# Performance work log

Hardware: AMD Instinct MI355X
Metric: run time of the kernel (lower is better)

The kernel has to match this reference:

```python
import jax, jax.numpy as jnp
import numpy as np

N_NODES = 16000
N_EDGES = 128000
IN_FEAT = 1024   # nb_iprs
OUT_FEAT = 1024  # RelGraphConv out / embed_dim
N_RELS = 7
NB_GOS = 4096


def setup_inputs() -> dict:
    key = jax.random.key(0)
    ks = jax.random.split(key, 9)
    feat = jax.random.normal(ks[0], (N_NODES, IN_FEAT), dtype=jnp.float32)
    src = jax.random.randint(ks[1], (N_EDGES,), 0, N_NODES, dtype=jnp.int32)
    dst = jax.random.randint(ks[2], (N_EDGES,), 0, N_NODES, dtype=jnp.int32)
    etypes = jax.random.randint(ks[3], (N_EDGES,), 0, N_RELS, dtype=jnp.int32)
    # RelGraphConv params (regularizer=None): per-relation weight, self-loop weight, bias
    s = 1.0 / np.sqrt(IN_FEAT)
    W_rel = jax.random.uniform(ks[4], (N_RELS, IN_FEAT, OUT_FEAT), dtype=jnp.float32, minval=-s, maxval=s)
    W_loop = jax.random.uniform(ks[5], (IN_FEAT, OUT_FEAT), dtype=jnp.float32, minval=-s, maxval=s)
    bias = jnp.zeros((OUT_FEAT,), dtype=jnp.float32)
    # GO embeddings, init U(-k, k) with k = sqrt(1/embed_dim)
    k = 1.0 / np.sqrt(OUT_FEAT)
    go_embed = jax.random.uniform(ks[6], (NB_GOS, OUT_FEAT), dtype=jnp.float32, minval=-k, maxval=k)
    go_rad = jax.random.uniform(ks[7], (NB_GOS, 1), dtype=jnp.float32, minval=-k, maxval=k)
    return {"feat": feat, "src": src, "dst": dst, "etypes": etypes,
            "W_rel": W_rel, "W_loop": W_loop, "bias": bias,
            "go_embed": go_embed, "go_rad": go_rad}


def reference(feat, src, dst, etypes, W_rel, W_loop, bias, go_embed, go_rad):
    n = feat.shape[0]
    # RelGraphConv (sum aggregation, self-loop, bias, no activation):
    # message on edge e: feat[src[e]] @ W_rel[etypes[e]]; by linearity, first
    # segment-sum source features per (dst, rel), then one batched GEMM.
    x_src = feat[src]                                   # [E, in]
    seg = dst.astype(jnp.int32) * N_RELS + etypes       # combined (dst, rel) id
    agg = jax.ops.segment_sum(x_src, seg, num_segments=n * N_RELS)
    agg = agg.reshape(n, N_RELS, IN_FEAT)               # [N, R, in]
    h = jnp.einsum('nri,rio->no', agg, W_rel) + feat @ W_loop + bias  # [N, out]
    # scoring: sigmoid(x @ E_go^T + |rad|)
    logits = jax.nn.sigmoid(h @ go_embed.T + jnp.abs(go_rad).reshape(1, -1))
    return logits
```

## Files before the change

kernel.cpp:

```cpp
#include <hip/hip_runtime.h>
#include <math.h>

#define N_NODES 16000
#define N_EDGES 128000
#define KDIM 1024
#define N_RELS 7
#define NB_GOS 4096
#define KCAT (KDIM * (N_RELS + 1))
#define MPAD 16128

#define BM 128
#define BN 128
#define BK 32
#define CAP2 (N_EDGES + N_RELS * BM)
#define NTILE_E (CAP2 / BM)

typedef __attribute__((ext_vector_type(8))) short bf16x8;
typedef __attribute__((ext_vector_type(8))) unsigned short u16x8;
typedef __attribute__((ext_vector_type(4))) float f32x4;

__device__ __forceinline__ unsigned short f2bf(float f) {
    union { float f; unsigned int u; } v; v.f = f;
    unsigned int u = v.u + 0x7FFFu + ((v.u >> 16) & 1u);
    return (unsigned short)(u >> 16);
}

__device__ __forceinline__ void gload16(const void* g, void* lds) {
    __builtin_amdgcn_global_load_lds(
        (const __attribute__((address_space(1))) unsigned int*)g,
        (__attribute__((address_space(3))) unsigned int*)lds, 16, 0, 0);
}

__device__ __forceinline__ void wg_barrier() {
    __builtin_amdgcn_sched_barrier(0);
    asm volatile("s_barrier" ::: "memory");
    __builtin_amdgcn_sched_barrier(0);
}


__global__ __launch_bounds__(256) void conv_bf16(const float* __restrict__ in,
                                                 unsigned short* __restrict__ out, int n8) {
    int i = blockIdx.x * 256 + threadIdx.x;
    if (i >= n8) return;
    const float4* in4 = (const float4*)in;
    float4 x = in4[2 * i], y = in4[2 * i + 1];
    u16x8 o;
    o[0] = f2bf(x.x); o[1] = f2bf(x.y); o[2] = f2bf(x.z); o[3] = f2bf(x.w);
    o[4] = f2bf(y.x); o[5] = f2bf(y.y); o[6] = f2bf(y.z); o[7] = f2bf(y.w);
    *(u16x8*)&out[(size_t)i * 8] = o;
}

__global__ __launch_bounds__(256) void conv_cat(const float* __restrict__ in,
                                                unsigned short* __restrict__ Acat) {
    int i = blockIdx.x * 256 + threadIdx.x;
    if (i >= N_NODES * (KDIM / 8)) return;
    int n = i >> 7, c8 = (i & 127) * 8;
    const float4* in4 = (const float4*)(in + (size_t)n * KDIM + c8);
    float4 x = in4[0], y = in4[1];
    u16x8 o;
    o[0] = f2bf(x.x); o[1] = f2bf(x.y); o[2] = f2bf(x.z); o[3] = f2bf(x.w);
    o[4] = f2bf(y.x); o[5] = f2bf(y.y); o[6] = f2bf(y.z); o[7] = f2bf(y.w);
    *(u16x8*)&Acat[(size_t)n * KCAT + c8] = o;
}

__global__ void transpose_w(const float* __restrict__ Wrel,
                            const float* __restrict__ Wloop,
                            unsigned short* __restrict__ WrelT,
                            unsigned short* __restrict__ WloopT) {
    __shared__ float t[32][33];
    int z = blockIdx.z;
    const float* src = (z < N_RELS) ? Wrel + (size_t)z * KDIM * KDIM : Wloop;
    unsigned short* dst = (z < N_RELS) ? WrelT + (size_t)z * KDIM * KDIM : WloopT;
    int tx = threadIdx.x, ty = threadIdx.y;
    int x = blockIdx.x * 32 + tx;
    int y0 = blockIdx.y * 32;
    #pragma unroll
    for (int j = 0; j < 4; j++)
        t[ty + 8 * j][tx] = src[(size_t)(y0 + ty + 8 * j) * KDIM + x];
    __syncthreads();
    #pragma unroll
    for (int j = 0; j < 4; j++) {
        int n = blockIdx.x * 32 + ty + 8 * j;
        dst[(size_t)n * KDIM + y0 + tx] = f2bf(t[tx][ty + 8 * j]);
    }
}

__global__ void transpose_cat(const float* __restrict__ Wrel,
                              const float* __restrict__ Wloop,
                              unsigned short* __restrict__ BT) {
    __shared__ float t[32][33];
    int z = blockIdx.z;
    const float* src = (z == 0) ? Wloop : Wrel + (size_t)(z - 1) * KDIM * KDIM;
    int tx = threadIdx.x, ty = threadIdx.y;
    int x = blockIdx.x * 32 + tx;
    int y0 = blockIdx.y * 32;
    #pragma unroll
    for (int j = 0; j < 4; j++)
        t[ty + 8 * j][tx] = src[(size_t)(y0 + ty + 8 * j) * KDIM + x];
    __syncthreads();
    #pragma unroll
    for (int j = 0; j < 4; j++) {
        int o = blockIdx.x * 32 + ty + 8 * j;
        BT[(size_t)o * KCAT + z * KDIM + y0 + tx] = f2bf(t[tx][ty + 8 * j]);
    }
}


__global__ void zero_ints(int* p, int n) {
    int i = blockIdx.x * 256 + threadIdx.x;
    if (i < n) p[i] = 0;
}

__global__ void hist_dst(const int* __restrict__ dst, int* cnt) {
    int e = blockIdx.x * 256 + threadIdx.x;
    if (e < N_EDGES) atomicAdd(&cnt[dst[e]], 1);
}

__global__ __launch_bounds__(1024) void scan_offs(const int* __restrict__ cnt,
                                                  int* __restrict__ offs) {
    __shared__ int part[1024];
    int t = threadIdx.x;
    int base = t * 16;
    int local[16];
    int s = 0;
    if (base < N_NODES) {
        #pragma unroll
        for (int j = 0; j < 16; j++) { local[j] = cnt[base + j]; s += local[j]; }
    }
    part[t] = s;
    __syncthreads();
    for (int d = 1; d < 1024; d <<= 1) {
        int v = (t >= d) ? part[t - d] : 0;
        __syncthreads();
        part[t] += v;
        __syncthreads();
    }
    if (base < N_NODES) {
        int ex = (t == 0) ? 0 : part[t - 1];
        #pragma unroll
        for (int j = 0; j < 16; j++) { offs[base + j] = ex; ex += local[j]; }
        if (base + 16 == N_NODES) offs[N_NODES] = ex;
    }
}

__global__ void scatter_dst(const int* __restrict__ src, const int* __restrict__ dst,
                            const int* __restrict__ et, const int* __restrict__ offs,
                            int* cursor, int* __restrict__ se) {
    int e = blockIdx.x * 256 + threadIdx.x;
    if (e < N_EDGES) {
        int d = dst[e];
        int p = atomicAdd(&cursor[d], 1);
        se[offs[d] + p] = (src[e] << 3) | et[e];
    }
}

__global__ __launch_bounds__(256) void aggregate(const float* __restrict__ feat,
                                                 const int* __restrict__ offs,
                                                 const int* __restrict__ se,
                                                 unsigned short* __restrict__ Acat) {
    int n = blockIdx.x;
    int t = threadIdx.x;
    int e0 = offs[n], e1 = offs[n + 1];
    float4 a0 = {0,0,0,0}, a1 = a0, a2 = a0, a3 = a0, a4 = a0, a5 = a0, a6 = a0;
    const float4* f4 = (const float4*)feat;
    for (int i = e0; i < e1; i++) {
        int v = se[i];
        int s = v >> 3, r = v & 7;
        float4 x = f4[(size_t)s * (KDIM / 4) + t];
        #define ADD4(a) { a.x += x.x; a.y += x.y; a.z += x.z; a.w += x.w; }
        switch (r) {
            case 0: ADD4(a0) break; case 1: ADD4(a1) break;
            case 2: ADD4(a2) break; case 3: ADD4(a3) break;
            case 4: ADD4(a4) break; case 5: ADD4(a5) break;
            default: ADD4(a6) break;
        }
        #undef ADD4
    }
    unsigned short* row = Acat + (size_t)n * KCAT + KDIM;
    #define ST4(rr, a) { ushort4 o; o.x = f2bf(a.x); o.y = f2bf(a.y); \
                         o.z = f2bf(a.z); o.w = f2bf(a.w); \
                         *(ushort4*)(row + rr * KDIM + t * 4) = o; }
    ST4(0, a0) ST4(1, a1) ST4(2, a2) ST4(3, a3) ST4(4, a4) ST4(5, a5) ST4(6, a6)
    #undef ST4
}


template<int MODE>
__global__ __launch_bounds__(512, 2) void gemm256(
    const unsigned short* __restrict__ A,
    const unsigned short* __restrict__ BT,
    const float* __restrict__ br,
    float* __restrict__ out, int kd)
{
    __shared__ unsigned short As[2][256 * 64];
    __shared__ unsigned short Bs[2][256 * 64];

    const int tid = threadIdx.x;
    const int l = tid & 63, w = tid >> 6;
    const int wm = w >> 2, wn = w & 3;

    const int nwg = gridDim.x * gridDim.y;
    const int b = blockIdx.y * gridDim.x + blockIdx.x;
    const int q8 = nwg >> 3, r8 = nwg & 7;
    const int xcd = b & 7, idx = b >> 3;
    const int wg = (xcd < r8 ? xcd * (q8 + 1) : r8 * (q8 + 1) + (xcd - r8) * q8) + idx;
    const int m0 = (wg / gridDim.x) * 256;
    const int n0 = (wg % gridDim.x) * 256;

    const int NT = kd >> 6;

    const int rr = tid >> 3;
    const int cc = (tid & 7) ^ (rr & 7);

    auto stageA = [&](int dbuf, int kt, int half) {
        #pragma unroll
        for (int j = 0; j < 2; j++) {
            unsigned short* lp = &As[dbuf][(size_t)(w * 8 + j * 128 + half * 64) * 64];
            const unsigned short* gp = A + (size_t)(m0 + rr + j * 128 + half * 64) * kd
                                         + kt * 64 + cc * 8;
            gload16(gp, lp);
        }
    };
    auto stageB = [&](int dbuf, int kt, int half) {
        #pragma unroll
        for (int j = 0; j < 2; j++) {
            unsigned short* lp = &Bs[dbuf][(size_t)(w * 8 + j * 64 + half * 128) * 64];
            const unsigned short* gp = BT + (size_t)(n0 + rr + j * 64 + half * 128) * kd
                                          + kt * 64 + cc * 8;
            gload16(gp, lp);
        }
    };

    stageB(0, 0, 0); stageA(0, 0, 0); stageB(0, 0, 1); stageA(0, 0, 1);
    if (NT > 1) {
        stageB(1, 1, 0); stageA(1, 1, 0); stageB(1, 1, 1);
        asm volatile("s_waitcnt vmcnt(6)" ::: "memory");
    } else {
        asm volatile("s_waitcnt vmcnt(0)" ::: "memory");
    }
    wg_barrier();

    f32x4 acc[8][4] = {};

    for (int t = 0; t < NT; t++) {
        const int buf = t & 1;
        bf16x8 bfr[4][2];
        #pragma unroll
        for (int q = 0; q < 4; q++) {
            bf16x8 afr[2][2];
            if (q == 0) {
                #pragma unroll
                for (int nj = 0; nj < 4; nj++)
                    #pragma unroll
                    for (int ks = 0; ks < 2; ks++) {
                        int row = wn * 64 + nj * 16 + (l & 15);
                        int ch = (ks * 4 + (l >> 4)) ^ (l & 7);
                        bfr[nj][ks] = *(const bf16x8*)&Bs[buf][row * 64 + ch * 8];
                    }
            }
            #pragma unroll
            for (int i = 0; i < 2; i++)
                #pragma unroll
                for (int ks = 0; ks < 2; ks++) {
                    int row = wm * 128 + (2 * q + i) * 16 + (l & 15);
                    int ch = (ks * 4 + (l >> 4)) ^ (l & 7);
                    afr[i][ks] = *(const bf16x8*)&As[buf][row * 64 + ch * 8];
                }
            if (q == 0)      { if (t + 1 < NT) stageA(buf ^ 1, t + 1, 1); }
            else if (q == 1) { if (t + 2 < NT) stageB(buf, t + 2, 0); }
            else if (q == 2) { if (t + 2 < NT) stageA(buf, t + 2, 0); }
            else             { if (t + 2 < NT) stageB(buf, t + 2, 1); }
            wg_barrier();
            __builtin_amdgcn_s_setprio(1);
            #pragma unroll
            for (int i = 0; i < 2; i++)
                #pragma unroll
                for (int nj = 0; nj < 4; nj++)
                    #pragma unroll
                    for (int ks = 0; ks < 2; ks++)
                        acc[2 * q + i][nj] = __builtin_amdgcn_mfma_f32_16x16x32_bf16(
                            afr[i][ks], bfr[nj][ks], acc[2 * q + i][nj], 0, 0, 0);
            __builtin_amdgcn_s_setprio(0);
            if (q == 3) {
                if (t + 2 < NT) asm volatile("s_waitcnt vmcnt(6)" ::: "memory");
                else            asm volatile("s_waitcnt vmcnt(0)" ::: "memory");
            }
            wg_barrier();
        }
    }

    const int cl = l & 15, rh = (l >> 4) * 4;
    float brv[4];
    #pragma unroll
    for (int nj = 0; nj < 4; nj++) brv[nj] = br[n0 + wn * 64 + nj * 16 + cl];
    #pragma unroll
    for (int mi = 0; mi < 8; mi++) {
        #pragma unroll
        for (int r4 = 0; r4 < 4; r4++) {
            const int row = m0 + wm * 128 + mi * 16 + rh + r4;
            if (MODE == 2 && row >= N_NODES) continue;
            #pragma unroll
            for (int nj = 0; nj < 4; nj++) {
                const int col = n0 + wn * 64 + nj * 16 + cl;
                float x = acc[mi][nj][r4];
                if (MODE == 0) {
                    out[(size_t)row * KDIM + col] = x + brv[nj];
                } else {
                    x += fabsf(brv[nj]);
                    out[(size_t)row * (size_t)NB_GOS + col] = 1.0f / (1.0f + __expf(-x));
                }
            }
        }
    }
}


__global__ void init_buckets(int* cnt, int* cursor, int* bucket) {
    int i = blockIdx.x * 256 + threadIdx.x;
    if (i < 8) { cnt[i] = 0; cursor[i] = 0; }
    if (i < CAP2) bucket[i] = -1;
}

__global__ __launch_bounds__(256) void count_etypes(const int* __restrict__ et, int* cnt) {
    __shared__ int lc[N_RELS];
    if (threadIdx.x < N_RELS) lc[threadIdx.x] = 0;
    __syncthreads();
    int e = blockIdx.x * 256 + threadIdx.x;
    if (e < N_EDGES) atomicAdd(&lc[et[e]], 1);
    __syncthreads();
    if (threadIdx.x < N_RELS) atomicAdd(&cnt[threadIdx.x], lc[threadIdx.x]);
}

__global__ void calc_offsets(const int* __restrict__ cnt, int* offs) {
    if (blockIdx.x == 0 && threadIdx.x == 0) {
        int acc = 0;
        offs[0] = 0;
        for (int r = 0; r < N_RELS; r++) {
            acc += ((cnt[r] + BM - 1) / BM) * BM;
            offs[r + 1] = acc;
        }
    }
}

__global__ __launch_bounds__(256) void scatter_edges(const int* __restrict__ et,
                                                     const int* __restrict__ offs,
                                                     int* cursor, int* bucket) {
    __shared__ int lc[N_RELS];
    __shared__ int lbase[N_RELS];
    if (threadIdx.x < N_RELS) lc[threadIdx.x] = 0;
    __syncthreads();
    int e = blockIdx.x * 256 + threadIdx.x;
    int r = 0, my = 0;
    bool valid = (e < N_EDGES);
    if (valid) { r = et[e]; my = atomicAdd(&lc[r], 1); }
    __syncthreads();
    if (threadIdx.x < N_RELS)
        lbase[threadIdx.x] = atomicAdd(&cursor[threadIdx.x], lc[threadIdx.x]);
    __syncthreads();
    if (valid) bucket[offs[r] + lbase[r] + my] = e;
}

template<int MODE>
__global__ __launch_bounds__(256) void mfma_gemm(
    const unsigned short* __restrict__ A,
    const unsigned short* __restrict__ BT,
    const float* __restrict__ br,
    float* __restrict__ out,
    const int* __restrict__ src,
    const int* __restrict__ dst,
    const int* __restrict__ bucket,
    const int* __restrict__ offs,
    int kd)
{
    __shared__ unsigned short As[BM * BK];
    __shared__ unsigned short Bs[BN * BK];
    __shared__ int s_src[BM];
    __shared__ int s_dst[BM];

    const int tid = threadIdx.x;
    const int l = tid & 63;
    const int w = tid >> 6;
    const int wr = w >> 1, wc = w & 1;

    const int nwg = gridDim.x * gridDim.y;
    const int b = blockIdx.y * gridDim.x + blockIdx.x;
    const int cpx = nwg >> 3;
    const int swz = (b & 7) * cpx + (b >> 3);
    const int n0 = (swz / gridDim.y) * BN;
    const int m0 = (swz % gridDim.y) * BM;

    const unsigned short* Bb = BT;
    if (MODE == 1) {
        int rel = -1;
        #pragma unroll
        for (int q = 0; q < N_RELS; q++)
            if (m0 >= offs[q] && m0 < offs[q + 1]) rel = q;
        if (rel < 0) return;
        Bb = BT + (size_t)rel * KDIM * KDIM;
        if (tid < BM) {
            int e = bucket[m0 + tid];
            s_src[tid] = (e >= 0) ? src[e] : -1;
            s_dst[tid] = (e >= 0) ? dst[e] : -1;
        }
        __syncthreads();
    }

    f32x4 acc[4][4] = {};

    const int s0 = tid, s1 = tid + 256;
    const int r0 = s0 >> 2, kc0 = (s0 & 3) * 8;
    const int r1 = s1 >> 2, kc1 = (s1 & 3) * 8;
    unsigned short* ldsA0 = As + (w * 64) * 8;
    unsigned short* ldsA1 = As + (w * 64 + 256) * 8;
    unsigned short* ldsB0 = Bs + (w * 64) * 8;
    unsigned short* ldsB1 = Bs + (w * 64 + 256) * 8;

    size_t arow0, arow1;
    if (MODE == 1) {
        int sr0 = s_src[r0]; arow0 = (sr0 < 0) ? 0 : (size_t)sr0;
        int sr1 = s_src[r1]; arow1 = (sr1 < 0) ? 0 : (size_t)sr1;
    } else {
        arow0 = (size_t)(m0 + r0);
        arow1 = (size_t)(m0 + r1);
    }
    const size_t brow0 = (size_t)(n0 + r0), brow1 = (size_t)(n0 + r1);

    const int fa = (wr * 64 + (l & 15)) * BK + (l >> 4) * 8;
    const int fb = (wc * 64 + (l & 15)) * BK + (l >> 4) * 8;

    for (int k0 = 0; k0 < kd; k0 += BK) {
        gload16(A + arow0 * kd + k0 + kc0, ldsA0);
        gload16(A + arow1 * kd + k0 + kc1, ldsA1);
        gload16(Bb + brow0 * kd + k0 + kc0, ldsB0);
        gload16(Bb + brow1 * kd + k0 + kc1, ldsB1);
        __syncthreads();

        bf16x8 a[4], bfr[4];
        #pragma unroll
        for (int mi = 0; mi < 4; mi++)
            a[mi] = *(const bf16x8*)&As[fa + mi * 16 * BK];
        #pragma unroll
        for (int nj = 0; nj < 4; nj++)
            bfr[nj] = *(const bf16x8*)&Bs[fb + nj * 16 * BK];
        #pragma unroll
        for (int mi = 0; mi < 4; mi++)
            #pragma unroll
            for (int nj = 0; nj < 4; nj++)
                acc[mi][nj] = __builtin_amdgcn_mfma_f32_16x16x32_bf16(a[mi], bfr[nj], acc[mi][nj], 0, 0, 0);
        __syncthreads();
    }

    const int cl = l & 15, rh = (l >> 4) * 4;
    #pragma unroll
    for (int mi = 0; mi < 4; mi++) {
        #pragma unroll
        for (int r4 = 0; r4 < 4; r4++) {
            const int row = wr * 64 + mi * 16 + rh + r4;
            if (MODE == 1) {
                const int d = s_dst[row];
                if (d >= 0) {
                    #pragma unroll
                    for (int nj = 0; nj < 4; nj++) {
                        const int col = n0 + wc * 64 + nj * 16 + cl;
                        atomicAdd(&out[(size_t)d * KDIM + col], acc[mi][nj][r4]);
                    }
                }
            } else if (MODE == 0) {
                #pragma unroll
                for (int nj = 0; nj < 4; nj++) {
                    const int col = n0 + wc * 64 + nj * 16 + cl;
                    out[(size_t)(m0 + row) * KDIM + col] = acc[mi][nj][r4] + br[col];
                }
            } else {
                #pragma unroll
                for (int nj = 0; nj < 4; nj++) {
                    const int col = n0 + wc * 64 + nj * 16 + cl;
                    float x = acc[mi][nj][r4] + fabsf(br[col]);
                    out[(size_t)(m0 + row) * (size_t)NB_GOS + col] = 1.0f / (1.0f + expf(-x));
                }
            }
        }
    }
}


extern "C" void kernel_launch(void* const* d_in, const int* in_sizes, int n_in,
                              void* d_out, int out_size, void* d_ws, size_t ws_size,
                              hipStream_t stream) {
    const float* feat   = (const float*)d_in[0];
    const int*   src    = (const int*)d_in[1];
    const int*   dst    = (const int*)d_in[2];
    const int*   etypes = (const int*)d_in[3];
    const float* W_rel  = (const float*)d_in[4];
    const float* W_loop = (const float*)d_in[5];
    const float* bias   = (const float*)d_in[6];
    const float* go_emb = (const float*)d_in[7];
    const float* go_rad = (const float*)d_in[8];
    float* out = (float*)d_out;

    const size_t ACAT_B = (size_t)MPAD * KCAT * 2;
    const size_t H_B    = (size_t)MPAD * KDIM * 4;
    const size_t BTC_B  = (size_t)KDIM * KCAT * 2;
    const size_t GOB_B  = (size_t)NB_GOS * KDIM * 2;
    const size_t CNT_B  = 16384 * 4;
    const size_t NEED   = ACAT_B + H_B + BTC_B + GOB_B + 3 * CNT_B + (size_t)N_EDGES * 4;

    if (ws_size >= NEED) {
        char* p = (char*)d_ws;
        unsigned short* Acat  = (unsigned short*)p;  p += ACAT_B;
        float*          h     = (float*)p;           p += H_B;
        unsigned short* BTcat = (unsigned short*)p;  p += BTC_B;
        unsigned short* gob   = (unsigned short*)p;  p += GOB_B;
        int* cnt    = (int*)p;                       p += CNT_B;
        int* cursor = (int*)p;                       p += CNT_B;
        int* offs   = (int*)p;                       p += CNT_B;
        int* se     = (int*)p;
        unsigned short* hb = (unsigned short*)d_ws;

        zero_ints<<<(2 * 16384 + 255) / 256, 256, 0, stream>>>(cnt, 2 * 16384);
        conv_cat<<<(N_NODES * (KDIM / 8) + 255) / 256, 256, 0, stream>>>(feat, Acat);
        conv_bf16<<<(NB_GOS * KDIM / 8 + 255) / 256, 256, 0, stream>>>(go_emb, gob, NB_GOS * KDIM / 8);
        {
            dim3 g(KDIM / 32, KDIM / 32, N_RELS + 1), bb(32, 8);
            transpose_cat<<<g, bb, 0, stream>>>(W_rel, W_loop, BTcat);
        }
        hist_dst<<<(N_EDGES + 255) / 256, 256, 0, stream>>>(dst, cnt);
        scan_offs<<<1, 1024, 0, stream>>>(cnt, offs);
        scatter_dst<<<(N_EDGES + 255) / 256, 256, 0, stream>>>(src, dst, etypes, offs, cursor, se);
        aggregate<<<N_NODES, 256, 0, stream>>>(feat, offs, se, Acat);

        {
            dim3 g(KDIM / 256, MPAD / 256);
            gemm256<0><<<g, 512, 0, stream>>>(Acat, BTcat, bias, h, KCAT);
        }
        conv_bf16<<<(N_NODES * KDIM / 8 + 255) / 256, 256, 0, stream>>>(h, hb, N_NODES * KDIM / 8);
        {
            dim3 g(NB_GOS / 256, MPAD / 256);
            gemm256<2><<<g, 512, 0, stream>>>(hb, gob, go_rad, out, KDIM);
        }
        return;
    }

    char* p = (char*)d_ws;
    float* h            = (float*)p;            p += (size_t)N_NODES * KDIM * 4;
    unsigned short* fb  = (unsigned short*)p;   p += (size_t)N_NODES * KDIM * 2;
    unsigned short* wrT = (unsigned short*)p;   p += (size_t)N_RELS * KDIM * KDIM * 2;
    unsigned short* wlT = (unsigned short*)p;   p += (size_t)KDIM * KDIM * 2;
    unsigned short* gob = (unsigned short*)p;   p += (size_t)NB_GOS * KDIM * 2;
    int* cnt    = (int*)p;
    int* cursor = cnt + 8;
    int* offs   = cursor + 8;
    int* bucket = offs + 16;

    conv_bf16<<<(N_NODES * KDIM / 8 + 255) / 256, 256, 0, stream>>>(feat, fb, N_NODES * KDIM / 8);
    conv_bf16<<<(NB_GOS * KDIM / 8 + 255) / 256, 256, 0, stream>>>(go_emb, gob, NB_GOS * KDIM / 8);
    {
        dim3 g(KDIM / 32, KDIM / 32, N_RELS + 1), bb(32, 8);
        transpose_w<<<g, bb, 0, stream>>>(W_rel, W_loop, wrT, wlT);
    }
    init_buckets<<<(CAP2 + 255) / 256, 256, 0, stream>>>(cnt, cursor, bucket);
    count_etypes<<<(N_EDGES + 255) / 256, 256, 0, stream>>>(etypes, cnt);
    calc_offsets<<<1, 64, 0, stream>>>(cnt, offs);
    scatter_edges<<<(N_EDGES + 255) / 256, 256, 0, stream>>>(etypes, offs, cursor, bucket);
    {
        dim3 g(KDIM / BN, N_NODES / BM);
        mfma_gemm<0><<<g, 256, 0, stream>>>(fb, wlT, bias, h, nullptr, nullptr, nullptr, nullptr, KDIM);
    }
    {
        dim3 g(KDIM / BN, NTILE_E);
        mfma_gemm<1><<<g, 256, 0, stream>>>(fb, wrT, nullptr, h, src, dst, bucket, offs, KDIM);
    }
    conv_bf16<<<(N_NODES * KDIM / 8 + 255) / 256, 256, 0, stream>>>(h, fb, N_NODES * KDIM / 8);
    {
        dim3 g(NB_GOS / BN, N_NODES / BM);
        mfma_gemm<2><<<g, 256, 0, stream>>>(fb, gob, go_rad, out, nullptr, nullptr, nullptr, nullptr, KDIM);
    }
}
```

Baseline: 681.0 us.

## Restructure GEMM main loop into eight quadrant phases and fuse bf16 epilogue

Rewrites the gemm256 main loop to process two K-tiles per iteration in eight phases, each computing one 64x32 quadrant of the warp tile with interleaved async global->LDS staging and a changed B-tile row mapping. It also makes the first GEMM write its output directly as bf16, which removes the separate fp32 h buffer and the conv_bf16 pass. The finer phasing aims to overlap loads with MFMA more evenly, at the cost of more barriers and an assumption that NT is even. The epilogue fusion saves a full read/write of h.

```diff
diff --git a/kernel.cpp b/kernel.cpp
--- a/kernel.cpp
+++ b/kernel.cpp
@@ -29,12 +29,6 @@
     __builtin_amdgcn_global_load_lds(
         (const __attribute__((address_space(1))) unsigned int*)g,
         (__attribute__((address_space(3))) unsigned int*)lds, 16, 0, 0);
-}
-
-__device__ __forceinline__ void wg_barrier() {
-    __builtin_amdgcn_sched_barrier(0);
-    asm volatile("s_barrier" ::: "memory");
-    __builtin_amdgcn_sched_barrier(0);
 }
 
 
@@ -190,7 +184,7 @@
     const unsigned short* __restrict__ A,
     const unsigned short* __restrict__ BT,
     const float* __restrict__ br,
-    float* __restrict__ out, int kd)
+    void* __restrict__ outv, int kd)
 {
     __shared__ unsigned short As[2][256 * 64];
     __shared__ unsigned short Bs[2][256 * 64];
@@ -198,6 +192,7 @@
     const int tid = threadIdx.x;
     const int l = tid & 63, w = tid >> 6;
     const int wm = w >> 2, wn = w & 3;
+    const int lrow = l & 15, lhi = l >> 4, lx = l & 7;
 
     const int nwg = gridDim.x * gridDim.y;
     const int b = blockIdx.y * gridDim.x + blockIdx.x;
@@ -208,6 +203,7 @@
     const int n0 = (wg % gridDim.x) * 256;
 
     const int NT = kd >> 6;
+    const int NI = NT >> 1;
 
     const int rr = tid >> 3;
     const int cc = (tid & 7) ^ (rr & 7);
@@ -224,70 +220,74 @@
     auto stageB = [&](int dbuf, int kt, int half) {
         #pragma unroll
         for (int j = 0; j < 2; j++) {
-            unsigned short* lp = &Bs[dbuf][(size_t)(w * 8 + j * 64 + half * 128) * 64];
-            const unsigned short* gp = BT + (size_t)(n0 + rr + j * 64 + half * 128) * kd
+            const int brow = (w & 3) * 8 + (w >> 2) * 64 + j * 128 + half * 32;
+            unsigned short* lp = &Bs[dbuf][(size_t)brow * 64];
+            const unsigned short* gp = BT + (size_t)(n0 + (rr & 31) + (rr >> 5) * 64
+                                                     + j * 128 + half * 32) * kd
                                           + kt * 64 + cc * 8;
             gload16(gp, lp);
         }
     };
 
-    stageB(0, 0, 0); stageA(0, 0, 0); stageB(0, 0, 1); stageA(0, 0, 1);
-    if (NT > 1) {
-        stageB(1, 1, 0); stageA(1, 1, 0); stageB(1, 1, 1);
-        asm volatile("s_waitcnt vmcnt(6)" ::: "memory");
-    } else {
-        asm volatile("s_waitcnt vmcnt(0)" ::: "memory");
-    }
-    wg_barrier();
+    stageA(0, 0, 0); stageB(0, 0, 0); stageA(0, 0, 1); stageB(0, 0, 1);
+    stageA(1, 1, 0); stageB(1, 1, 0);
+    asm volatile("s_waitcnt vmcnt(4)" ::: "memory");
+    __builtin_amdgcn_s_barrier();
 
     f32x4 acc[8][4] = {};
 
-    for (int t = 0; t < NT; t++) {
-        const int buf = t & 1;
-        bf16x8 bfr[4][2];
-        #pragma unroll
-        for (int q = 0; q < 4; q++) {
-            bf16x8 afr[2][2];
-            if (q == 0) {
-                #pragma unroll
-                for (int nj = 0; nj < 4; nj++)
-                    #pragma unroll
-                    for (int ks = 0; ks < 2; ks++) {
-                        int row = wn * 64 + nj * 16 + (l & 15);
-                        int ch = (ks * 4 + (l >> 4)) ^ (l & 7);
-                        bfr[nj][ks] = *(const bf16x8*)&Bs[buf][row * 64 + ch * 8];
-                    }
-            }
-            #pragma unroll
-            for (int i = 0; i < 2; i++)
-                #pragma unroll
-                for (int ks = 0; ks < 2; ks++) {
-                    int row = wm * 128 + (2 * q + i) * 16 + (l & 15);
-                    int ch = (ks * 4 + (l >> 4)) ^ (l & 7);
-                    afr[i][ks] = *(const bf16x8*)&As[buf][row * 64 + ch * 8];
-                }
-            if (q == 0)      { if (t + 1 < NT) stageA(buf ^ 1, t + 1, 1); }
-            else if (q == 1) { if (t + 2 < NT) stageB(buf, t + 2, 0); }
-            else if (q == 2) { if (t + 2 < NT) stageA(buf, t + 2, 0); }
-            else             { if (t + 2 < NT) stageB(buf, t + 2, 1); }
-            wg_barrier();
-            __builtin_amdgcn_s_setprio(1);
-            #pragma unroll
-            for (int i = 0; i < 2; i++)
-                #pragma unroll
-                for (int nj = 0; nj < 4; nj++)
-                    #pragma unroll
-                    for (int ks = 0; ks < 2; ks++)
-                        acc[2 * q + i][nj] = __builtin_amdgcn_mfma_f32_16x16x32_bf16(
-                            afr[i][ks], bfr[nj][ks], acc[2 * q + i][nj], 0, 0, 0);
-            __builtin_amdgcn_s_setprio(0);
-            if (q == 3) {
-                if (t + 2 < NT) asm volatile("s_waitcnt vmcnt(6)" ::: "memory");
-                else            asm volatile("s_waitcnt vmcnt(0)" ::: "memory");
-            }
-            wg_barrier();
-        }
-    }
+#define PH(BUF, MH, NH, STG, WT) do {                                         \
+    bf16x8 afr[4][2], bfr[2][2];                                              \
+    _Pragma("unroll")                                                         \
+    for (int mi = 0; mi < 4; mi++) {                                          \
+        _Pragma("unroll")                                                     \
+        for (int ks = 0; ks < 2; ks++) {                                      \
+            const int row = wm * 128 + (MH) * 64 + mi * 16 + lrow;            \
+            const int ch = (ks * 4 + lhi) ^ lx;                               \
+            afr[mi][ks] = *(const bf16x8*)&As[BUF][row * 64 + ch * 8];        \
+        } }                                                                   \
+    _Pragma("unroll")                                                         \
+    for (int nj = 0; nj < 2; nj++) {                                          \
+        _Pragma("unroll")                                                     \
+        for (int ks = 0; ks < 2; ks++) {                                      \
+            const int row = wn * 64 + (NH) * 32 + nj * 16 + lrow;             \
+            const int ch = (ks * 4 + lhi) ^ lx;                               \
+            bfr[nj][ks] = *(const bf16x8*)&Bs[BUF][row * 64 + ch * 8];        \
+        } }                                                                   \
+    STG;                                                                      \
+    __builtin_amdgcn_s_barrier();                                             \
+    asm volatile("s_waitcnt lgkmcnt(0)");                                     \
+    __builtin_amdgcn_s_setprio(1);                                            \
+    _Pragma("unroll")                                                         \
+    for (int mi = 0; mi < 4; mi++) {                                          \
+        _Pragma("unroll")                                                     \
+        for (int nj = 0; nj < 2; nj++) {                                      \
+            _Pragma("unroll")                                                 \
+            for (int ks = 0; ks < 2; ks++)                                    \
+                acc[(MH)*4+mi][(NH)*2+nj] = __builtin_amdgcn_mfma_f32_16x16x32_bf16( \
+                    afr[mi][ks], bfr[nj][ks], acc[(MH)*4+mi][(NH)*2+nj], 0, 0, 0);   \
+        } }                                                                   \
+    __builtin_amdgcn_s_setprio(0);                                            \
+    WT;                                                                       \
+    __builtin_amdgcn_s_barrier();                                             \
+} while (0)
+
+    for (int t = 0; t < NI; t++) {
+        const bool nl = (t + 1 < NI);
+        PH(0, 0, 0, stageA(1, 2*t+1, 1), ((void)0));
+        PH(0, 0, 1, stageB(1, 2*t+1, 1), ((void)0));
+        PH(0, 1, 0, if (nl) stageA(0, 2*t+2, 0), ((void)0));
+        PH(0, 1, 1, if (nl) stageB(0, 2*t+2, 0),
+           if (nl) { asm volatile("s_waitcnt vmcnt(4)" ::: "memory"); }
+           else    { asm volatile("s_waitcnt vmcnt(0)" ::: "memory"); });
+        PH(1, 0, 0, if (nl) stageA(0, 2*t+2, 1), ((void)0));
+        PH(1, 0, 1, if (nl) stageB(0, 2*t+2, 1), ((void)0));
+        PH(1, 1, 0, if (nl) stageA(1, 2*t+3, 0), ((void)0));
+        PH(1, 1, 1, if (nl) stageB(1, 2*t+3, 0),
+           if (nl) { asm volatile("s_waitcnt vmcnt(4)" ::: "memory"); }
+           else    { asm volatile("s_waitcnt vmcnt(0)" ::: "memory"); });
+    }
+#undef PH
 
     const int cl = l & 15, rh = (l >> 4) * 4;
     float brv[4];
@@ -304,10 +304,11 @@
                 const int col = n0 + wn * 64 + nj * 16 + cl;
                 float x = acc[mi][nj][r4];
                 if (MODE == 0) {
-                    out[(size_t)row * KDIM + col] = x + brv[nj];
+                    ((unsigned short*)outv)[(size_t)row * KDIM + col] = f2bf(x + brv[nj]);
                 } else {
                     x += fabsf(brv[nj]);
-                    out[(size_t)row * (size_t)NB_GOS + col] = 1.0f / (1.0f + __expf(-x));
+                    ((float*)outv)[(size_t)row * (size_t)NB_GOS + col] =
+                        1.0f / (1.0f + __expf(-x));
                 }
             }
         }
@@ -499,23 +500,22 @@
     float* out = (float*)d_out;
 
     const size_t ACAT_B = (size_t)MPAD * KCAT * 2;
-    const size_t H_B    = (size_t)MPAD * KDIM * 4;
+    const size_t HB_B   = (size_t)MPAD * KDIM * 2;
     const size_t BTC_B  = (size_t)KDIM * KCAT * 2;
     const size_t GOB_B  = (size_t)NB_GOS * KDIM * 2;
     const size_t CNT_B  = 16384 * 4;
-    const size_t NEED   = ACAT_B + H_B + BTC_B + GOB_B + 3 * CNT_B + (size_t)N_EDGES * 4;
+    const size_t NEED   = ACAT_B + HB_B + BTC_B + GOB_B + 3 * CNT_B + (size_t)N_EDGES * 4;
 
     if (ws_size >= NEED) {
         char* p = (char*)d_ws;
         unsigned short* Acat  = (unsigned short*)p;  p += ACAT_B;
-        float*          h     = (float*)p;           p += H_B;
+        unsigned short* hb    = (unsigned short*)p;  p += HB_B;
         unsigned short* BTcat = (unsigned short*)p;  p += BTC_B;
         unsigned short* gob   = (unsigned short*)p;  p += GOB_B;
         int* cnt    = (int*)p;                       p += CNT_B;
         int* cursor = (int*)p;                       p += CNT_B;
         int* offs   = (int*)p;                       p += CNT_B;
         int* se     = (int*)p;
-        unsigned short* hb = (unsigned short*)d_ws;
 
         zero_ints<<<(2 * 16384 + 255) / 256, 256, 0, stream>>>(cnt, 2 * 16384);
         conv_cat<<<(N_NODES * (KDIM / 8) + 255) / 256, 256, 0, stream>>>(feat, Acat);
@@ -531,9 +531,8 @@
 
         {
             dim3 g(KDIM / 256, MPAD / 256);
-            gemm256<0><<<g, 512, 0, stream>>>(Acat, BTcat, bias, h, KCAT);
-        }
-        conv_bf16<<<(N_NODES * KDIM / 8 + 255) / 256, 256, 0, stream>>>(h, hb, N_NODES * KDIM / 8);
+            gemm256<0><<<g, 512, 0, stream>>>(Acat, BTcat, bias, hb, KCAT);
+        }
         {
             dim3 g(NB_GOS / 256, MPAD / 256);
             gemm256<2><<<g, 512, 0, stream>>>(hb, gob, go_rad, out, KDIM);
```

New measurement: 683.6 us. Within noise of the previous version (+0.4%).
